# Optimization experiments

Measured on AMD Instinct MI355X. Metric: run time of the kernel, lower is better.

The kernel has to match this reference:

```python
import jax, jax.numpy as jnp
import numpy as np

KP_VARIANCE = 0.01  # init kwarg: kp_variance (float -> plain Gaussian branch)


def make_coordinate_grid(h, w, dtype):
    # torch make_coordinate_grid: x,y in [-1,1], last dim is (x, y)
    x = jnp.linspace(-1.0, 1.0, w, dtype=dtype)
    y = jnp.linspace(-1.0, 1.0, h, dtype=dtype)
    gx, gy = jnp.meshgrid(x, y)  # each (h, w)
    return jnp.stack([gx, gy], axis=-1)  # (h, w, 2)


def grid_sample_bilinear(img, coords):
    """F.grid_sample, bilinear, zeros padding, align_corners=True.
    img: (bs, C, H, W); coords: (bs, d, K, h, w, 2) with (x, y) in [-1,1].
    Returns (bs, d, K, C, h, w)."""
    bs, C, H, W = img.shape
    x = (coords[..., 0] + 1.0) * (W - 1) / 2.0
    y = (coords[..., 1] + 1.0) * (H - 1) / 2.0
    x0 = jnp.floor(x); y0 = jnp.floor(y)
    x1 = x0 + 1.0;     y1 = y0 + 1.0
    wx1 = x - x0; wx0 = 1.0 - wx1
    wy1 = y - y0; wy0 = 1.0 - wy1

    def corner(ix, iy, wgt):
        valid = (ix >= 0) & (ix <= W - 1) & (iy >= 0) & (iy <= H - 1)
        ixc = jnp.clip(ix, 0, W - 1).astype(jnp.int32)
        iyc = jnp.clip(iy, 0, H - 1).astype(jnp.int32)
        # per-batch gather: im (C,H,W), yy/xx (d,K,h,w) -> (C,d,K,h,w)
        vals = jax.vmap(lambda im, yy, xx: im[:, yy, xx])(img, iyc, ixc)  # (bs,C,d,K,h,w)
        w_eff = (wgt * valid.astype(img.dtype))[:, None]  # (bs,1,d,K,h,w)
        return vals * w_eff

    out = (corner(x0, y0, wx0 * wy0) + corner(x1, y0, wx1 * wy0)
           + corner(x0, y1, wx0 * wy1) + corner(x1, y1, wx1 * wy1))
    return jnp.transpose(out, (0, 2, 3, 1, 4, 5))  # (bs,d,K,C,h,w)


def setup_inputs() -> dict:
    key = jax.random.key(0)
    k1, k2, k3 = jax.random.split(key, 3)
    bs, d, K, C, h, w = 4, 16, 10, 3, 128, 128
    kp_appearance_mean = jax.random.uniform(k1, (bs, 1, K, 2), jnp.float32) * 2.0 - 1.0
    kp_video_mean = jax.random.uniform(k2, (bs, d, K, 2), jnp.float32) * 2.0 - 1.0
    appearance_frame = jax.random.normal(k3, (bs, C, 1, h, w), jnp.float32)
    return {"kp_appearance_mean": kp_appearance_mean,
            "kp_video_mean": kp_video_mean,
            "appearance_frame": appearance_frame}


def reference(kp_appearance_mean, kp_video_mean, appearance_frame):
    bs, C, _, h, w = appearance_frame.shape
    _, d, K, _ = kp_video_mean.shape
    dtype = appearance_frame.dtype

    # combine_kp (difference_type='absolute', float kp_variance)
    diff = kp_video_mean - kp_video_mean[:, 0:1]          # (bs,d,K,2)
    kp_mean = diff + kp_appearance_mean                    # (bs,d,K,2)
    kp_video_diff = -diff                                  # (bs,d,K,2)

    grid = make_coordinate_grid(h, w, dtype)               # (h,w,2)

    # use_heatmap: kp2gaussian then subtract first frame
    mean_sub = grid - kp_mean[:, :, :, None, None, :]      # (bs,d,K,h,w,2)
    heatmap = jnp.exp(-0.5 * jnp.sum(mean_sub * mean_sub, axis=-1) / KP_VARIANCE)
    heatmap = heatmap - heatmap[:, 0:1]
    heatmap = heatmap[:, :, :, None]                       # (bs,d,K,1,h,w)

    # use_difference: broadcast diff over spatial dims
    diff_maps = jnp.broadcast_to(kp_video_diff[:, :, :, :, None, None],
                                 (bs, d, K, 2, h, w))

    # use_deformed_appearance: grid_sample of appearance frame by shifted grid
    deformation = grid + kp_video_diff[:, :, :, None, None, :]  # (bs,d,K,h,w,2)
    img = appearance_frame[:, :, 0]                              # (bs,C,h,w)
    deformed = grid_sample_bilinear(img, deformation)            # (bs,d,K,C,h,w)

    enc = jnp.concatenate([heatmap, diff_maps, deformed], axis=3)  # (bs,d,K,1+2+C,h,w)
    enc = enc.reshape(bs, d, -1, h, w)
    return jnp.transpose(enc, (0, 2, 1, 3, 4))  # (bs, (3+C)*K, d, h, w)
```

## Files before the change

### kernel.cpp

```cpp
#include <hip/hip_runtime.h>

#define BS 4
#define DD 16
#define KK 10
#define CC 3
#define HH 128
#define WW 128

#define NROWS 9
#define LROW 132

__global__ __launch_bounds__(256) void movement_embed_kernel(
    const float* __restrict__ kp_app,
    const float* __restrict__ kp_vid,
    const float* __restrict__ img,
    float* __restrict__ out)
{
    __shared__ __align__(16) float P[CC][NROWS][LROW];

    const unsigned bi  = blockIdx.x;
    const unsigned sub = bi & 15u;
    const unsigned bdk = bi >> 4;
    const unsigned k   = bdk % KK;
    const unsigned t2  = bdk / KK;
    const unsigned d   = t2 % DD;
    const unsigned b   = t2 / DD;
    const int tid  = (int)threadIdx.x;
    const int lane = tid & 63;
    const int wv   = tid >> 6;

    const float kvx  = kp_vid[((b*DD + d)*KK + k)*2 + 0];
    const float kvy  = kp_vid[((b*DD + d)*KK + k)*2 + 1];
    const float kv0x = kp_vid[((b*DD + 0)*KK + k)*2 + 0];
    const float kv0y = kp_vid[((b*DD + 0)*KK + k)*2 + 1];
    const float kax  = kp_app[(b*KK + k)*2 + 0];
    const float kay  = kp_app[(b*KK + k)*2 + 1];

    const float diffx = kvx - kv0x;
    const float diffy = kvy - kv0y;
    const float mx = diffx + kax;
    const float my = diffy + kay;
    const float vdx = -diffx;
    const float vdy = -diffy;

    const float cx = vdx * 63.5f;
    const float cy = vdy * 63.5f;
    const float fcx = floorf(cx);
    const float fcy = floorf(cy);
    const int icx = (int)fcx;
    const int icy = (int)fcy;
    const float wx1 = cx - fcx, wx0 = 1.0f - wx1;
    const float wy1 = cy - fcy, wy0 = 1.0f - wy1;

    const int R0 = (int)(sub * 8u) + icy;
    const float* imgb = img + (size_t)b * (CC*HH*WW);

#pragma unroll
    for (int c = 0; c < CC; ++c) {
        const float* pc = imgb + c * (HH * WW);
#pragma unroll
        for (int ri = 0; ri < NROWS; ++ri) {
            if (((c * NROWS + ri) & 3) == wv) {
                const int  r   = R0 + ri;
                const bool rok = (unsigned)r < (unsigned)HH;
                const float* rp = pc + (size_t)min(max(r, 0), HH - 1) * WW;

                const int c0 = icx + lane;
                const int c1 = c0 + 64;
                float v0 = rp[min(max(c0, 0), WW - 1)];
                float v1 = rp[min(max(c1, 0), WW - 1)];
                v0 = (rok && (unsigned)c0 < (unsigned)WW) ? v0 : 0.0f;
                v1 = (rok && (unsigned)c1 < (unsigned)WW) ? v1 : 0.0f;
                P[c][ri][lane]      = v0;
                P[c][ri][lane + 64] = v1;
                if (lane == 0) {
                    const int c2 = icx + 128;
                    float v2 = rp[min(max(c2, 0), WW - 1)];
                    P[c][ri][128] = (rok && (unsigned)c2 < (unsigned)WW) ? v2 : 0.0f;
                }
            }
        }
    }
    __syncthreads();

    const int xg = tid & 31;
    const int ly = tid >> 5;
    const int x4 = xg * 4;
    const int y  = (int)(sub * 8u) + ly;

    const float step = 2.0f / 127.0f;
    const float gy  = (float)y  * step - 1.0f;
    const float gx0 = (float)x4 * step - 1.0f;

    const float dy1 = gy - my, dy0 = gy - kay;
    const float dy1sq = dy1 * dy1, dy0sq = dy0 * dy0;
    float hv[4];
#pragma unroll
    for (int j = 0; j < 4; ++j) {
        const float gx = gx0 + (float)j * step;
        const float dx1 = gx - mx, dx0 = gx - kax;
        hv[j] = __expf(-50.0f * (dx1 * dx1 + dy1sq))
              - __expf(-50.0f * (dx0 * dx0 + dy0sq));
    }

    float4 dvc[CC];
#pragma unroll
    for (int c = 0; c < CC; ++c) {
        const float* row0 = &P[c][ly][x4];
        const float* row1 = &P[c][ly + 1][x4];
        const float4 A = *(const float4*)row0;
        const float  ea = row0[4];
        const float4 B = *(const float4*)row1;
        const float  eb = row1[4];
        const float h0x = wx0 * A.x + wx1 * A.y;
        const float h0y = wx0 * A.y + wx1 * A.z;
        const float h0z = wx0 * A.z + wx1 * A.w;
        const float h0w = wx0 * A.w + wx1 * ea;
        const float h1x = wx0 * B.x + wx1 * B.y;
        const float h1y = wx0 * B.y + wx1 * B.z;
        const float h1z = wx0 * B.z + wx1 * B.w;
        const float h1w = wx0 * B.w + wx1 * eb;
        dvc[c] = make_float4(wy0 * h0x + wy1 * h1x,
                             wy0 * h0y + wy1 * h1y,
                             wy0 * h0z + wy1 * h1z,
                             wy0 * h0w + wy1 * h1w);
    }

    const size_t chs  = (size_t)DD * HH * WW;
    const size_t base = ((((size_t)b * (KK * 6) + k * 6) * DD + d) * HH + y) * WW + (size_t)x4;

    *(float4*)(out + base)         = make_float4(hv[0], hv[1], hv[2], hv[3]);
    *(float4*)(out + base + chs)   = make_float4(vdx, vdx, vdx, vdx);
    *(float4*)(out + base + 2*chs) = make_float4(vdy, vdy, vdy, vdy);
#pragma unroll
    for (int c = 0; c < CC; ++c)
        *(float4*)(out + base + (size_t)(3 + c) * chs) = dvc[c];
}

extern "C" void kernel_launch(void* const* d_in, const int* in_sizes, int n_in,
                              void* d_out, int out_size, void* d_ws, size_t ws_size,
                              hipStream_t stream) {
    const float* kp_app = (const float*)d_in[0];
    const float* kp_vid = (const float*)d_in[1];
    const float* img    = (const float*)d_in[2];
    float* out = (float*)d_out;

    const int nblocks = BS * DD * KK * 16;
    movement_embed_kernel<<<nblocks, 256, 0, stream>>>(kp_app, kp_vid, img, out);
}
```

Baseline: 250.5 us.

## Give each wavefront private LDS rows to drop block barrier

Each wavefront now loads its own three image rows per channel into a private LDS slice and computes its two output rows from them, so the block-wide __syncthreads is removed. Only an lgkmcnt wait is used before reading LDS. The heatmap and diff stores are issued before that wait so they overlap the row loads. The cost is redundant global reads, 12 rows per channel instead of 9, and a larger LDS footprint.

New measurement: 242.8 us (median of 2 runs). 3.1% less time.

```diff
diff --git a/kernel.cpp b/kernel.cpp
--- a/kernel.cpp
+++ b/kernel.cpp
@@ -7,8 +7,9 @@
 #define HH 128
 #define WW 128
 
-#define NROWS 9
 #define LROW 132
+
+using f4 = __attribute__((ext_vector_type(4))) float;
 
 __global__ __launch_bounds__(256) void movement_embed_kernel(
     const float* __restrict__ kp_app,
@@ -16,7 +17,7 @@
     const float* __restrict__ img,
     float* __restrict__ out)
 {
-    __shared__ __align__(16) float P[CC][NROWS][LROW];
+    __shared__ __align__(16) float P[4][CC][3][LROW];
 
     const unsigned bi  = blockIdx.x;
     const unsigned sub = bi & 15u;
@@ -52,41 +53,43 @@
     const float wx1 = cx - fcx, wx0 = 1.0f - wx1;
     const float wy1 = cy - fcy, wy0 = 1.0f - wy1;
 
-    const int R0 = (int)(sub * 8u) + icy;
+    const int R0 = (int)(sub * 8u) + 2 * wv + icy;
     const float* imgb = img + (size_t)b * (CC*HH*WW);
 
 #pragma unroll
     for (int c = 0; c < CC; ++c) {
         const float* pc = imgb + c * (HH * WW);
 #pragma unroll
-        for (int ri = 0; ri < NROWS; ++ri) {
-            if (((c * NROWS + ri) & 3) == wv) {
-                const int  r   = R0 + ri;
-                const bool rok = (unsigned)r < (unsigned)HH;
-                const float* rp = pc + (size_t)min(max(r, 0), HH - 1) * WW;
+        for (int ri = 0; ri < 3; ++ri) {
+            const int  r   = R0 + ri;
+            const bool rok = (unsigned)r < (unsigned)HH;
+            const float* rp = pc + (size_t)min(max(r, 0), HH - 1) * WW;
 
-                const int c0 = icx + lane;
-                const int c1 = c0 + 64;
-                float v0 = rp[min(max(c0, 0), WW - 1)];
-                float v1 = rp[min(max(c1, 0), WW - 1)];
-                v0 = (rok && (unsigned)c0 < (unsigned)WW) ? v0 : 0.0f;
-                v1 = (rok && (unsigned)c1 < (unsigned)WW) ? v1 : 0.0f;
-                P[c][ri][lane]      = v0;
-                P[c][ri][lane + 64] = v1;
-                if (lane == 0) {
-                    const int c2 = icx + 128;
-                    float v2 = rp[min(max(c2, 0), WW - 1)];
-                    P[c][ri][128] = (rok && (unsigned)c2 < (unsigned)WW) ? v2 : 0.0f;
-                }
-            }
+            const int c0 = icx + lane;
+            const int c1 = c0 + 64;
+            float v0 = rp[min(max(c0, 0), WW - 1)];
+            float v1 = rp[min(max(c1, 0), WW - 1)];
+            v0 = (rok && (unsigned)c0 < (unsigned)WW) ? v0 : 0.0f;
+            v1 = (rok && (unsigned)c1 < (unsigned)WW) ? v1 : 0.0f;
+            P[wv][c][ri][lane]      = v0;
+            P[wv][c][ri][lane + 64] = v1;
         }
     }
-    __syncthreads();
+    if (lane < CC * 3) {
+        const int  c   = lane / 3;
+        const int  ri  = lane - c * 3;
+        const int  r   = R0 + ri;
+        const bool rok = (unsigned)r < (unsigned)HH;
+        const float* rp = imgb + c * (HH * WW) + (size_t)min(max(r, 0), HH - 1) * WW;
+        const int  c2  = icx + 128;
+        float v2 = rp[min(max(c2, 0), WW - 1)];
+        P[wv][c][ri][128] = (rok && (unsigned)c2 < (unsigned)WW) ? v2 : 0.0f;
+    }
 
-    const int xg = tid & 31;
-    const int ly = tid >> 5;
+    const int xg = lane & 31;
+    const int lr = lane >> 5;
     const int x4 = xg * 4;
-    const int y  = (int)(sub * 8u) + ly;
+    const int y  = (int)(sub * 8u) + 2 * wv + lr;
 
     const float step = 2.0f / 127.0f;
     const float gy  = (float)y  * step - 1.0f;
@@ -103,11 +106,24 @@
               - __expf(-50.0f * (dx0 * dx0 + dy0sq));
     }
 
-    float4 dvc[CC];
+    const size_t chs  = (size_t)DD * HH * WW;
+    const size_t base = ((((size_t)b * (KK * 6) + k * 6) * DD + d) * HH + y) * WW + (size_t)x4;
+
+    {
+        f4 h; h.x = hv[0]; h.y = hv[1]; h.z = hv[2]; h.w = hv[3];
+        *(f4*)(out + base) = h;
+        f4 vx; vx.x = vdx; vx.y = vdx; vx.z = vdx; vx.w = vdx;
+        *(f4*)(out + base + chs) = vx;
+        f4 vy; vy.x = vdy; vy.y = vdy; vy.z = vdy; vy.w = vdy;
+        *(f4*)(out + base + 2 * chs) = vy;
+    }
+
+    asm volatile("s_waitcnt lgkmcnt(0)" ::: "memory");
+
 #pragma unroll
     for (int c = 0; c < CC; ++c) {
-        const float* row0 = &P[c][ly][x4];
-        const float* row1 = &P[c][ly + 1][x4];
+        const float* row0 = &P[wv][c][lr][x4];
+        const float* row1 = &P[wv][c][lr + 1][x4];
         const float4 A = *(const float4*)row0;
         const float  ea = row0[4];
         const float4 B = *(const float4*)row1;
@@ -120,21 +136,13 @@
         const float h1y = wx0 * B.y + wx1 * B.z;
         const float h1z = wx0 * B.z + wx1 * B.w;
         const float h1w = wx0 * B.w + wx1 * eb;
-        dvc[c] = make_float4(wy0 * h0x + wy1 * h1x,
-                             wy0 * h0y + wy1 * h1y,
-                             wy0 * h0z + wy1 * h1z,
-                             wy0 * h0w + wy1 * h1w);
+        f4 dv;
+        dv.x = wy0 * h0x + wy1 * h1x;
+        dv.y = wy0 * h0y + wy1 * h1y;
+        dv.z = wy0 * h0z + wy1 * h1z;
+        dv.w = wy0 * h0w + wy1 * h1w;
+        *(f4*)(out + base + (size_t)(3 + c) * chs) = dv;
     }
-
-    const size_t chs  = (size_t)DD * HH * WW;
-    const size_t base = ((((size_t)b * (KK * 6) + k * 6) * DD + d) * HH + y) * WW + (size_t)x4;
-
-    *(float4*)(out + base)         = make_float4(hv[0], hv[1], hv[2], hv[3]);
-    *(float4*)(out + base + chs)   = make_float4(vdx, vdx, vdx, vdx);
-    *(float4*)(out + base + 2*chs) = make_float4(vdy, vdy, vdy, vdy);
-#pragma unroll
-    for (int c = 0; c < CC; ++c)
-        *(float4*)(out + base + (size_t)(3 + c) * chs) = dvc[c];
 }
 
 extern "C" void kernel_launch(void* const* d_in, const int* in_sizes, int n_in,
```

## Drop LDS staging; read bilinear taps directly from a padded workspace image copy

Applied to the files above, without the earlier changes.

Removes the shared-memory staging of image rows and the block barrier. Each thread now loads its bilinear taps straight from global memory (cache-served). A small pre-kernel copies the image into a workspace with guard padding so the out-of-range taps can be read unclamped and then masked. This cuts LDS traffic and the sync, at the cost of an extra kernel launch, a copy, and redundant global loads. It falls back to clamped loads if no workspace is available.

New measurement: 243.9 us. 1.03x faster.

```diff
diff --git a/kernel.cpp b/kernel.cpp
--- a/kernel.cpp
+++ b/kernel.cpp
@@ -6,18 +6,30 @@
 #define CC 3
 #define HH 128
 #define WW 128
+#define HW   (HH*WW)
+#define CHW  (CC*HW)
+#define IMG_FLOATS (BS*CHW)
+#define PAD_FLOATS 24576
+#define WS_NEED ((size_t)(IMG_FLOATS + 2*PAD_FLOATS) * 4)
 
-#define NROWS 9
-#define LROW 132
+using f4 = __attribute__((ext_vector_type(4))) float;
 
+struct F4U { float v[4]; };
+
+__global__ __launch_bounds__(256) void img_pad_copy(
+    const float* __restrict__ img, float* __restrict__ dst)
+{
+    const int i = (int)(blockIdx.x * 256u + threadIdx.x) * 4;
+    *(f4*)(dst + i) = *(const f4*)(img + i);
+}
+
+template<bool PADDED>
 __global__ __launch_bounds__(256) void movement_embed_kernel(
     const float* __restrict__ kp_app,
     const float* __restrict__ kp_vid,
-    const float* __restrict__ img,
+    const float* __restrict__ src,
     float* __restrict__ out)
 {
-    __shared__ __align__(16) float P[CC][NROWS][LROW];
-
     const unsigned bi  = blockIdx.x;
     const unsigned sub = bi & 15u;
     const unsigned bdk = bi >> 4;
@@ -25,9 +37,12 @@
     const unsigned t2  = bdk / KK;
     const unsigned d   = t2 % DD;
     const unsigned b   = t2 / DD;
-    const int tid  = (int)threadIdx.x;
-    const int lane = tid & 63;
-    const int wv   = tid >> 6;
+
+    const int tid = (int)threadIdx.x;
+    const int xg  = tid & 31;
+    const int ly  = tid >> 5;
+    const int x4  = xg * 4;
+    const int y   = (int)(sub * 8u) + ly;
 
     const float kvx  = kp_vid[((b*DD + d)*KK + k)*2 + 0];
     const float kvy  = kp_vid[((b*DD + d)*KK + k)*2 + 1];
@@ -45,96 +60,84 @@
 
     const float cx = vdx * 63.5f;
     const float cy = vdy * 63.5f;
-    const float fcx = floorf(cx);
-    const float fcy = floorf(cy);
-    const int icx = (int)fcx;
-    const int icy = (int)fcy;
+    const float fcx = floorf(cx), fcy = floorf(cy);
+    const int icx = (int)fcx, icy = (int)fcy;
     const float wx1 = cx - fcx, wx0 = 1.0f - wx1;
     const float wy1 = cy - fcy, wy0 = 1.0f - wy1;
 
-    const int R0 = (int)(sub * 8u) + icy;
-    const float* imgb = img + (size_t)b * (CC*HH*WW);
-
+    const int r0   = y + icy;
+    const int col0 = icx + x4;
+    const bool rv0 = (unsigned)r0       < (unsigned)HH;
+    const bool rv1 = (unsigned)(r0 + 1) < (unsigned)HH;
+    bool cv[5];
 #pragma unroll
-    for (int c = 0; c < CC; ++c) {
-        const float* pc = imgb + c * (HH * WW);
-#pragma unroll
-        for (int ri = 0; ri < NROWS; ++ri) {
-            if (((c * NROWS + ri) & 3) == wv) {
-                const int  r   = R0 + ri;
-                const bool rok = (unsigned)r < (unsigned)HH;
-                const float* rp = pc + (size_t)min(max(r, 0), HH - 1) * WW;
-
-                const int c0 = icx + lane;
-                const int c1 = c0 + 64;
-                float v0 = rp[min(max(c0, 0), WW - 1)];
-                float v1 = rp[min(max(c1, 0), WW - 1)];
-                v0 = (rok && (unsigned)c0 < (unsigned)WW) ? v0 : 0.0f;
-                v1 = (rok && (unsigned)c1 < (unsigned)WW) ? v1 : 0.0f;
-                P[c][ri][lane]      = v0;
-                P[c][ri][lane + 64] = v1;
-                if (lane == 0) {
-                    const int c2 = icx + 128;
-                    float v2 = rp[min(max(c2, 0), WW - 1)];
-                    P[c][ri][128] = (rok && (unsigned)c2 < (unsigned)WW) ? v2 : 0.0f;
-                }
-            }
-        }
-    }
-    __syncthreads();
-
-    const int xg = tid & 31;
-    const int ly = tid >> 5;
-    const int x4 = xg * 4;
-    const int y  = (int)(sub * 8u) + ly;
+    for (int e = 0; e < 5; ++e) cv[e] = (unsigned)(col0 + e) < (unsigned)WW;
 
     const float step = 2.0f / 127.0f;
     const float gy  = (float)y  * step - 1.0f;
     const float gx0 = (float)x4 * step - 1.0f;
-
     const float dy1 = gy - my, dy0 = gy - kay;
     const float dy1sq = dy1 * dy1, dy0sq = dy0 * dy0;
-    float hv[4];
+    float hvv[4];
 #pragma unroll
     for (int j = 0; j < 4; ++j) {
         const float gx = gx0 + (float)j * step;
         const float dx1 = gx - mx, dx0 = gx - kax;
-        hv[j] = __expf(-50.0f * (dx1 * dx1 + dy1sq))
-              - __expf(-50.0f * (dx0 * dx0 + dy0sq));
+        hvv[j] = __expf(-50.0f * (dx1 * dx1 + dy1sq))
+               - __expf(-50.0f * (dx0 * dx0 + dy0sq));
     }
 
-    float4 dvc[CC];
+    const size_t chs  = (size_t)DD * HW;
+    const size_t base = ((((size_t)b * (KK * 6) + k * 6) * DD + d) * HH + y) * WW + (size_t)x4;
+
+    {
+        f4 H;  H.x = hvv[0]; H.y = hvv[1]; H.z = hvv[2]; H.w = hvv[3];
+        *(f4*)(out + base) = H;
+        f4 VX; VX.x = vdx; VX.y = vdx; VX.z = vdx; VX.w = vdx;
+        *(f4*)(out + base + chs) = VX;
+        f4 VY; VY.x = vdy; VY.y = vdy; VY.z = vdy; VY.w = vdy;
+        *(f4*)(out + base + 2 * chs) = VY;
+    }
+
 #pragma unroll
     for (int c = 0; c < CC; ++c) {
-        const float* row0 = &P[c][ly][x4];
-        const float* row1 = &P[c][ly + 1][x4];
-        const float4 A = *(const float4*)row0;
-        const float  ea = row0[4];
-        const float4 B = *(const float4*)row1;
-        const float  eb = row1[4];
-        const float h0x = wx0 * A.x + wx1 * A.y;
-        const float h0y = wx0 * A.y + wx1 * A.z;
-        const float h0z = wx0 * A.z + wx1 * A.w;
-        const float h0w = wx0 * A.w + wx1 * ea;
-        const float h1x = wx0 * B.x + wx1 * B.y;
-        const float h1y = wx0 * B.y + wx1 * B.z;
-        const float h1z = wx0 * B.z + wx1 * B.w;
-        const float h1w = wx0 * B.w + wx1 * eb;
-        dvc[c] = make_float4(wy0 * h0x + wy1 * h1x,
-                             wy0 * h0y + wy1 * h1y,
-                             wy0 * h0z + wy1 * h1z,
-                             wy0 * h0w + wy1 * h1w);
+        float a0[5], a1[5];
+        if constexpr (PADDED) {
+            const long idx = (long)b * CHW + (long)c * HW + (long)r0 * WW + (long)col0;
+            const float* p = src + idx;
+            const F4U A  = *(const F4U*)p;
+            const float a4 = p[4];
+            const F4U Bt = *(const F4U*)(p + WW);
+            const float b4 = p[WW + 4];
+#pragma unroll
+            for (int e = 0; e < 4; ++e) { a0[e] = A.v[e]; a1[e] = Bt.v[e]; }
+            a0[4] = a4; a1[4] = b4;
+        } else {
+            const int rc0 = min(max(r0, 0), HH - 1);
+            const int rc1 = min(max(r0 + 1, 0), HH - 1);
+            const int cb  = b * CHW + c * HW;
+#pragma unroll
+            for (int e = 0; e < 5; ++e) {
+                const int cc = min(max(col0 + e, 0), WW - 1);
+                a0[e] = src[cb + rc0 * WW + cc];
+                a1[e] = src[cb + rc1 * WW + cc];
+            }
+        }
+#pragma unroll
+        for (int e = 0; e < 5; ++e) {
+            a0[e] = (rv0 && cv[e]) ? a0[e] : 0.0f;
+            a1[e] = (rv1 && cv[e]) ? a1[e] : 0.0f;
+        }
+        float dvv[4];
+#pragma unroll
+        for (int e = 0; e < 4; ++e) {
+            const float h0 = wx0 * a0[e] + wx1 * a0[e + 1];
+            const float h1 = wx0 * a1[e] + wx1 * a1[e + 1];
+            dvv[e] = wy0 * h0 + wy1 * h1;
+        }
+        f4 DV; DV.x = dvv[0]; DV.y = dvv[1]; DV.z = dvv[2]; DV.w = dvv[3];
+        *(f4*)(out + base + (size_t)(3 + c) * chs) = DV;
     }
-
-    const size_t chs  = (size_t)DD * HH * WW;
-    const size_t base = ((((size_t)b * (KK * 6) + k * 6) * DD + d) * HH + y) * WW + (size_t)x4;
-
-    *(float4*)(out + base)         = make_float4(hv[0], hv[1], hv[2], hv[3]);
-    *(float4*)(out + base + chs)   = make_float4(vdx, vdx, vdx, vdx);
-    *(float4*)(out + base + 2*chs) = make_float4(vdy, vdy, vdy, vdy);
-#pragma unroll
-    for (int c = 0; c < CC; ++c)
-        *(float4*)(out + base + (size_t)(3 + c) * chs) = dvc[c];
 }
 
 extern "C" void kernel_launch(void* const* d_in, const int* in_sizes, int n_in,
@@ -146,5 +149,14 @@
     float* out = (float*)d_out;
 
     const int nblocks = BS * DD * KK * 16;
-    movement_embed_kernel<<<nblocks, 256, 0, stream>>>(kp_app, kp_vid, img, out);
+
+    if (d_ws != nullptr && ws_size >= WS_NEED) {
+        float* wimg = (float*)d_ws;
+        img_pad_copy<<<IMG_FLOATS / (256 * 4), 256, 0, stream>>>(img, wimg + PAD_FLOATS);
+        movement_embed_kernel<true><<<nblocks, 256, 0, stream>>>(
+            kp_app, kp_vid, wimg + PAD_FLOATS, out);
+    } else {
+        movement_embed_kernel<false><<<nblocks, 256, 0, stream>>>(
+            kp_app, kp_vid, img, out);
+    }
 }
```
